# Optimization experiments

Measured on AMD Instinct MI355X. Metric: run time of the kernel, lower is better.

Reference implementation:

```python
import jax, jax.numpy as jnp
import numpy as np

N_NODES = 100000
N_EDGES = 1600000
F_IN = 64
F_OUT = 64


def setup_inputs() -> dict:
    key = jax.random.key(0)
    k1, k2, k3 = jax.random.split(key, 3)
    x = jax.random.normal(k1, (1, 1, N_NODES, F_IN), dtype=jnp.float32)
    edge_index = jax.random.randint(k2, (2, N_EDGES), 0, N_NODES, dtype=jnp.int32)
    # xavier-init linear weight [F_IN, F_OUT], zero bias (xavier_zero_bias)
    scale = jnp.sqrt(2.0 / (F_IN + F_OUT)).astype(jnp.float32)
    weight = jax.random.normal(k3, (F_IN, F_OUT), dtype=jnp.float32) * scale
    bias = jnp.zeros((F_OUT,), dtype=jnp.float32)
    return {"x": x, "edge_index": edge_index, "weight": weight, "bias": bias}


def reference(x, edge_index, weight, bias):
    # x: [B, T, N, F_in]
    B, T, N, _ = x.shape
    # linear transform
    h = jnp.einsum('btnf,fo->btno', x, weight) + bias  # [B,T,N,F_out]
    # add self loops
    loops = jnp.arange(N, dtype=edge_index.dtype)
    src = jnp.concatenate([edge_index[0], loops])  # [E+N]
    dst = jnp.concatenate([edge_index[1], loops])  # [E+N]
    w = jnp.ones(src.shape[0], dtype=h.dtype)
    # symmetric GCN normalization: D^{-1/2} A D^{-1/2} (degree over dst)
    deg = jnp.zeros((N,), dtype=h.dtype).at[dst].add(w)
    inv_sqrt = jnp.clip(deg, 1e-9) ** -0.5
    norm = inv_sqrt[dst] * w * inv_sqrt[src]  # [E+N]
    # gather src features, scale by norm, scatter-add to dst
    msg = h[:, :, src, :] * norm[None, None, :, None]  # [B,T,E+N,F_out]
    out = jnp.zeros_like(h).at[:, :, dst, :].add(msg)  # [B,T,N,F_out]
    # GraphConvBase post: activation (gelu), dropout=0, norm=identity
    return jax.nn.gelu(out)
```

## Files before the change

### kernel.cpp

```cpp
#include <hip/hip_runtime.h>
#include <hip/hip_fp16.h>
#include <math.h>

#define N_NODES 100000
#define N_EDGES 1600000
#define F_DIM 64
#define BSH 9
#define BNODES 512
#define NBUCK ((N_NODES + BNODES - 1) / BNODES)
#define CAP 12288
#define EPT 32
#define TILE (256 * EPT)
#define P1B ((N_EDGES + TILE - 1) / TILE)
#define LINB ((N_NODES + 255) / 256)

__global__ __launch_bounds__(256) void fused1_k(const int* __restrict__ src,
                                                const int* __restrict__ dst,
                                                int* __restrict__ bcur,
                                                unsigned int* __restrict__ tmp,
                                                const float* __restrict__ x,
                                                const float* __restrict__ W,
                                                const float* __restrict__ bias,
                                                __half* __restrict__ h) {
    if (blockIdx.x < P1B) {
        __shared__ int lcnt[NBUCK];
        __shared__ int lbase[NBUCK];
        for (int i = threadIdx.x; i < NBUCK; i += 256) lcnt[i] = 0;
        __syncthreads();

        int4 sreg[EPT / 4], dreg[EPT / 4];
        int base4 = blockIdx.x * (TILE / 4);
#pragma unroll
        for (int j = 0; j < EPT / 4; ++j) {
            int i4 = base4 + j * 256 + threadIdx.x;
            if (i4 < N_EDGES / 4) {
                sreg[j] = ((const int4*)src)[i4];
                dreg[j] = ((const int4*)dst)[i4];
                atomicAdd(&lcnt[dreg[j].x >> BSH], 1);
                atomicAdd(&lcnt[dreg[j].y >> BSH], 1);
                atomicAdd(&lcnt[dreg[j].z >> BSH], 1);
                atomicAdd(&lcnt[dreg[j].w >> BSH], 1);
            } else {
                dreg[j].x = -1;
            }
        }
        __syncthreads();
        for (int b = threadIdx.x; b < NBUCK; b += 256) {
            int c = lcnt[b];
            lbase[b] = c ? atomicAdd(&bcur[b], c) : 0;
            lcnt[b] = 0;
        }
        __syncthreads();
#pragma unroll
        for (int j = 0; j < EPT / 4; ++j) {
            if (dreg[j].x >= 0) {
                int d, s, b, r;
                d = dreg[j].x; s = sreg[j].x; b = d >> BSH;
                r = atomicAdd(&lcnt[b], 1);
                tmp[(size_t)b * CAP + lbase[b] + r] = (unsigned int)s | ((unsigned int)(d & (BNODES - 1)) << 17);
                d = dreg[j].y; s = sreg[j].y; b = d >> BSH;
                r = atomicAdd(&lcnt[b], 1);
                tmp[(size_t)b * CAP + lbase[b] + r] = (unsigned int)s | ((unsigned int)(d & (BNODES - 1)) << 17);
                d = dreg[j].z; s = sreg[j].z; b = d >> BSH;
                r = atomicAdd(&lcnt[b], 1);
                tmp[(size_t)b * CAP + lbase[b] + r] = (unsigned int)s | ((unsigned int)(d & (BNODES - 1)) << 17);
                d = dreg[j].w; s = sreg[j].w; b = d >> BSH;
                r = atomicAdd(&lcnt[b], 1);
                tmp[(size_t)b * CAP + lbase[b] + r] = (unsigned int)s | ((unsigned int)(d & (BNODES - 1)) << 17);
            }
        }
    } else {
        __shared__ float Ws[F_DIM][F_DIM];
        __shared__ float bs[F_DIM];
        for (int i = threadIdx.x; i < F_DIM * F_DIM; i += 256) Ws[i >> 6][i & 63] = W[i];
        if (threadIdx.x < F_DIM) bs[threadIdx.x] = bias[threadIdx.x];
        __syncthreads();

        int n = (blockIdx.x - P1B) * 256 + threadIdx.x;
        if (n >= N_NODES) return;

        float xr[F_DIM];
        const float4* xp = (const float4*)(x + (size_t)n * F_DIM);
#pragma unroll
        for (int k4 = 0; k4 < 16; ++k4) {
            float4 v = xp[k4];
            xr[k4 * 4 + 0] = v.x; xr[k4 * 4 + 1] = v.y;
            xr[k4 * 4 + 2] = v.z; xr[k4 * 4 + 3] = v.w;
        }
        __half* hp = h + (size_t)n * F_DIM;
#pragma unroll 1
        for (int f0 = 0; f0 < F_DIM; f0 += 4) {
            float a0 = bs[f0 + 0], a1 = bs[f0 + 1], a2 = bs[f0 + 2], a3 = bs[f0 + 3];
#pragma unroll
            for (int k = 0; k < F_DIM; ++k) {
                float xv = xr[k];
                a0 += xv * Ws[k][f0 + 0];
                a1 += xv * Ws[k][f0 + 1];
                a2 += xv * Ws[k][f0 + 2];
                a3 += xv * Ws[k][f0 + 3];
            }
            union { __half2 h2[2]; float2 f2; } u;
            u.h2[0] = __floats2half2_rn(a0, a1);
            u.h2[1] = __floats2half2_rn(a2, a3);
            *((float2*)(hp + f0)) = u.f2;
        }
    }
}

__global__ __launch_bounds__(1024) void passB_k(const unsigned int* __restrict__ tmp,
                                                const int* __restrict__ bcur,
                                                unsigned int* __restrict__ esrc,
                                                unsigned int* __restrict__ rowinfo,
                                                float* __restrict__ inv) {
    __shared__ int cnt[BNODES];
    __shared__ int cur[BNODES];
    __shared__ int ls[BNODES];
    int b = blockIdx.x;
    int tid = threadIdx.x;
    int beg0 = b * CAP;
    int cntb = bcur[b];

    if (tid < BNODES) cnt[tid] = 0;
    __syncthreads();
    for (int i = tid; i < cntb; i += 1024)
        atomicAdd(&cnt[tmp[beg0 + i] >> 17], 1);
    __syncthreads();

    int a = 0;
    if (tid < BNODES) { a = cnt[tid]; ls[tid] = a; }
    __syncthreads();
    for (int off = 1; off < BNODES; off <<= 1) {
        int p = 0;
        if (tid < BNODES && tid >= off) p = ls[tid - off];
        __syncthreads();
        if (tid < BNODES) ls[tid] += p;
        __syncthreads();
    }
    if (tid < BNODES) {
        int p0 = beg0 + ls[tid] - a;
        cur[tid] = p0;
        int n = (b << BSH) + tid;
        if (n < N_NODES) {
            rowinfo[n] = (unsigned int)p0 | ((unsigned int)a << 22);
            inv[n] = rsqrtf((float)(a + 1));
        }
    }
    __syncthreads();

    for (int i = tid; i < cntb; i += 1024) {
        unsigned int v = tmp[beg0 + i];
        int pos = atomicAdd(&cur[v >> 17], 1);
        esrc[pos] = v & 0x1FFFFu;
    }
}

__device__ __forceinline__ float gelu1(float x) {
    float x3 = x * x * x;
    float t = tanhf(0.7978845608028654f * (x + 0.044715f * x3));
    return 0.5f * x * (1.0f + t);
}

__global__ __launch_bounds__(256) void gather_k(const __half* __restrict__ h,
                                                const float* __restrict__ inv,
                                                const unsigned int* __restrict__ rowinfo,
                                                const unsigned int* __restrict__ esrc,
                                                float* __restrict__ out, int N) {
    int n = blockIdx.x * 4 + (threadIdx.x >> 6);
    if (n >= N) return;
    int lane = threadIdx.x & 63;
    int eslot = lane >> 4;
    int fq = lane & 15;

    unsigned int ri = rowinfo[n];
    int beg = (int)(ri & 0x3FFFFFu);
    int deg = (int)(ri >> 22);

    float ax = 0.f, ay = 0.f, az = 0.f, aw = 0.f;
    int k = eslot;
    for (; k + 12 < deg; k += 16) {
        int s0 = (int)esrc[beg + k];
        int s1 = (int)esrc[beg + k + 4];
        int s2 = (int)esrc[beg + k + 8];
        int s3 = (int)esrc[beg + k + 12];
        float w0 = inv[s0], w1 = inv[s1], w2 = inv[s2], w3 = inv[s3];
        union { float2 f; __half2 h2[2]; } u0, u1, u2, u3;
        u0.f = *((const float2*)(h + (size_t)s0 * F_DIM) + fq);
        u1.f = *((const float2*)(h + (size_t)s1 * F_DIM) + fq);
        u2.f = *((const float2*)(h + (size_t)s2 * F_DIM) + fq);
        u3.f = *((const float2*)(h + (size_t)s3 * F_DIM) + fq);
        float2 a, b;
        a = __half22float2(u0.h2[0]); b = __half22float2(u0.h2[1]);
        ax = fmaf(a.x, w0, ax); ay = fmaf(a.y, w0, ay); az = fmaf(b.x, w0, az); aw = fmaf(b.y, w0, aw);
        a = __half22float2(u1.h2[0]); b = __half22float2(u1.h2[1]);
        ax = fmaf(a.x, w1, ax); ay = fmaf(a.y, w1, ay); az = fmaf(b.x, w1, az); aw = fmaf(b.y, w1, aw);
        a = __half22float2(u2.h2[0]); b = __half22float2(u2.h2[1]);
        ax = fmaf(a.x, w2, ax); ay = fmaf(a.y, w2, ay); az = fmaf(b.x, w2, az); aw = fmaf(b.y, w2, aw);
        a = __half22float2(u3.h2[0]); b = __half22float2(u3.h2[1]);
        ax = fmaf(a.x, w3, ax); ay = fmaf(a.y, w3, ay); az = fmaf(b.x, w3, az); aw = fmaf(b.y, w3, aw);
    }
    for (; k < deg; k += 4) {
        int s0 = (int)esrc[beg + k];
        float w0 = inv[s0];
        union { float2 f; __half2 h2[2]; } u0;
        u0.f = *((const float2*)(h + (size_t)s0 * F_DIM) + fq);
        float2 a = __half22float2(u0.h2[0]);
        float2 b = __half22float2(u0.h2[1]);
        ax = fmaf(a.x, w0, ax); ay = fmaf(a.y, w0, ay); az = fmaf(b.x, w0, az); aw = fmaf(b.y, w0, aw);
    }
    ax += __shfl_xor(ax, 16); ay += __shfl_xor(ay, 16);
    az += __shfl_xor(az, 16); aw += __shfl_xor(aw, 16);
    ax += __shfl_xor(ax, 32); ay += __shfl_xor(ay, 32);
    az += __shfl_xor(az, 32); aw += __shfl_xor(aw, 32);

    if (eslot == 0) {
        float invn = inv[n];
        union { float2 f; __half2 h2[2]; } us;
        us.f = *((const float2*)(h + (size_t)n * F_DIM) + fq);
        float2 s0 = __half22float2(us.h2[0]);
        float2 s1 = __half22float2(us.h2[1]);
        float4 o;
        o.x = gelu1((ax + s0.x * invn) * invn);
        o.y = gelu1((ay + s0.y * invn) * invn);
        o.z = gelu1((az + s1.x * invn) * invn);
        o.w = gelu1((aw + s1.y * invn) * invn);
        ((float4*)(out + (size_t)n * F_DIM))[fq] = o;
    }
}

extern "C" void kernel_launch(void* const* d_in, const int* in_sizes, int n_in,
                              void* d_out, int out_size, void* d_ws, size_t ws_size,
                              hipStream_t stream) {
    const float* x    = (const float*)d_in[0];
    const int*   ei   = (const int*)d_in[1];
    const float* W    = (const float*)d_in[2];
    const float* bias = (const float*)d_in[3];
    float* out = (float*)d_out;

    const int* src = ei;
    const int* dst = ei + N_EDGES;

    unsigned int* tmp     = (unsigned int*)d_ws;
    unsigned int* esrc    = tmp + (size_t)NBUCK * CAP;
    unsigned int* rowinfo = esrc + (size_t)NBUCK * CAP;
    float*        inv     = (float*)(rowinfo + N_NODES);
    int*          bcur    = (int*)(inv + N_NODES);
    size_t off = (size_t)(bcur + NBUCK) - (size_t)d_ws;
    off = (off + 31) & ~(size_t)31;
    __half* h = (__half*)((char*)d_ws + off);

    hipMemsetAsync(bcur, 0, NBUCK * sizeof(int), stream);

    fused1_k<<<P1B + LINB, 256, 0, stream>>>(src, dst, bcur, tmp, x, W, bias, h);
    passB_k<<<NBUCK, 1024, 0, stream>>>(tmp, bcur, esrc, rowinfo, inv);
    gather_k<<<(N_NODES + 3) / 4, 256, 0, stream>>>(h, inv, rowinfo, esrc, out, N_NODES);
}
```

Baseline: 113.8 us.

## Merge bucket-sort second pass into first kernel via grid-wide atomic barrier

```diff
diff --git a/kernel.cpp b/kernel.cpp
--- a/kernel.cpp
+++ b/kernel.cpp
@@ -13,26 +13,42 @@
 #define TILE (256 * EPT)
 #define P1B ((N_EDGES + TILE - 1) / TILE)
 #define LINB ((N_NODES + 255) / 256)
-
-__global__ __launch_bounds__(256) void fused1_k(const int* __restrict__ src,
-                                                const int* __restrict__ dst,
-                                                int* __restrict__ bcur,
-                                                unsigned int* __restrict__ tmp,
-                                                const float* __restrict__ x,
-                                                const float* __restrict__ W,
-                                                const float* __restrict__ bias,
-                                                __half* __restrict__ h) {
-    if (blockIdx.x < P1B) {
-        __shared__ int lcnt[NBUCK];
-        __shared__ int lbase[NBUCK];
-        for (int i = threadIdx.x; i < NBUCK; i += 256) lcnt[i] = 0;
+#define GRID (P1B + LINB)
+
+typedef float __attribute__((ext_vector_type(4))) f32x4;
+
+__global__ __launch_bounds__(256, 4) void fusedall_k(const int* __restrict__ src,
+                                                     const int* __restrict__ dst,
+                                                     int* __restrict__ bcur,
+                                                     unsigned int* __restrict__ tmp,
+                                                     const float* __restrict__ x,
+                                                     const float* __restrict__ W,
+                                                     const float* __restrict__ bias,
+                                                     __half* __restrict__ h,
+                                                     unsigned int* __restrict__ esrc,
+                                                     unsigned int* __restrict__ rowinfo,
+                                                     float* __restrict__ inv) {
+    __shared__ int lcnt[NBUCK];
+    __shared__ int lbase[NBUCK];
+    __shared__ float Ws[F_DIM][F_DIM];
+    __shared__ float bs[F_DIM];
+    __shared__ int cnt[BNODES];
+    __shared__ int cur[BNODES];
+    __shared__ int ls[256];
+
+    const int bid = blockIdx.x;
+    const int tid = threadIdx.x;
+    int* done = bcur + NBUCK;
+
+    if (bid < P1B) {
+        for (int i = tid; i < NBUCK; i += 256) lcnt[i] = 0;
         __syncthreads();
 
         int4 sreg[EPT / 4], dreg[EPT / 4];
-        int base4 = blockIdx.x * (TILE / 4);
+        int base4 = bid * (TILE / 4);
 #pragma unroll
         for (int j = 0; j < EPT / 4; ++j) {
-            int i4 = base4 + j * 256 + threadIdx.x;
+            int i4 = base4 + j * 256 + tid;
             if (i4 < N_EDGES / 4) {
                 sreg[j] = ((const int4*)src)[i4];
                 dreg[j] = ((const int4*)dst)[i4];
@@ -45,7 +61,7 @@
             }
         }
         __syncthreads();
-        for (int b = threadIdx.x; b < NBUCK; b += 256) {
+        for (int b = tid; b < NBUCK; b += 256) {
             int c = lcnt[b];
             lbase[b] = c ? atomicAdd(&bcur[b], c) : 0;
             lcnt[b] = 0;
@@ -70,87 +86,98 @@
             }
         }
     } else {
-        __shared__ float Ws[F_DIM][F_DIM];
-        __shared__ float bs[F_DIM];
-        for (int i = threadIdx.x; i < F_DIM * F_DIM; i += 256) Ws[i >> 6][i & 63] = W[i];
-        if (threadIdx.x < F_DIM) bs[threadIdx.x] = bias[threadIdx.x];
-        __syncthreads();
-
-        int n = (blockIdx.x - P1B) * 256 + threadIdx.x;
-        if (n >= N_NODES) return;
-
-        float xr[F_DIM];
-        const float4* xp = (const float4*)(x + (size_t)n * F_DIM);
-#pragma unroll
-        for (int k4 = 0; k4 < 16; ++k4) {
-            float4 v = xp[k4];
-            xr[k4 * 4 + 0] = v.x; xr[k4 * 4 + 1] = v.y;
-            xr[k4 * 4 + 2] = v.z; xr[k4 * 4 + 3] = v.w;
-        }
-        __half* hp = h + (size_t)n * F_DIM;
+        for (int i = tid; i < F_DIM * F_DIM; i += 256) Ws[i >> 6][i & 63] = W[i];
+        if (tid < F_DIM) bs[tid] = bias[tid];
+        __syncthreads();
+
+        int n = (bid - P1B) * 256 + tid;
+        if (n < N_NODES) {
+            float xr[F_DIM];
+            const float4* xp = (const float4*)(x + (size_t)n * F_DIM);
+#pragma unroll
+            for (int k4 = 0; k4 < 16; ++k4) {
+                float4 v = xp[k4];
+                xr[k4 * 4 + 0] = v.x; xr[k4 * 4 + 1] = v.y;
+                xr[k4 * 4 + 2] = v.z; xr[k4 * 4 + 3] = v.w;
+            }
+            __half* hp = h + (size_t)n * F_DIM;
 #pragma unroll 1
-        for (int f0 = 0; f0 < F_DIM; f0 += 4) {
-            float a0 = bs[f0 + 0], a1 = bs[f0 + 1], a2 = bs[f0 + 2], a3 = bs[f0 + 3];
-#pragma unroll
-            for (int k = 0; k < F_DIM; ++k) {
-                float xv = xr[k];
-                a0 += xv * Ws[k][f0 + 0];
-                a1 += xv * Ws[k][f0 + 1];
-                a2 += xv * Ws[k][f0 + 2];
-                a3 += xv * Ws[k][f0 + 3];
-            }
-            union { __half2 h2[2]; float2 f2; } u;
-            u.h2[0] = __floats2half2_rn(a0, a1);
-            u.h2[1] = __floats2half2_rn(a2, a3);
-            *((float2*)(hp + f0)) = u.f2;
-        }
-    }
-}
-
-__global__ __launch_bounds__(1024) void passB_k(const unsigned int* __restrict__ tmp,
-                                                const int* __restrict__ bcur,
-                                                unsigned int* __restrict__ esrc,
-                                                unsigned int* __restrict__ rowinfo,
-                                                float* __restrict__ inv) {
-    __shared__ int cnt[BNODES];
-    __shared__ int cur[BNODES];
-    __shared__ int ls[BNODES];
-    int b = blockIdx.x;
-    int tid = threadIdx.x;
-    int beg0 = b * CAP;
-    int cntb = bcur[b];
-
-    if (tid < BNODES) cnt[tid] = 0;
+            for (int f0 = 0; f0 < F_DIM; f0 += 4) {
+                float a0 = bs[f0 + 0], a1 = bs[f0 + 1], a2 = bs[f0 + 2], a3 = bs[f0 + 3];
+#pragma unroll
+                for (int k = 0; k < F_DIM; ++k) {
+                    float xv = xr[k];
+                    a0 += xv * Ws[k][f0 + 0];
+                    a1 += xv * Ws[k][f0 + 1];
+                    a2 += xv * Ws[k][f0 + 2];
+                    a3 += xv * Ws[k][f0 + 3];
+                }
+                union { __half2 h2[2]; float2 f2; } u;
+                u.h2[0] = __floats2half2_rn(a0, a1);
+                u.h2[1] = __floats2half2_rn(a2, a3);
+                *((float2*)(hp + f0)) = u.f2;
+            }
+        }
+    }
+
+    __threadfence();
     __syncthreads();
-    for (int i = tid; i < cntb; i += 1024)
-        atomicAdd(&cnt[tmp[beg0 + i] >> 17], 1);
+    if (tid == 0)
+        __hip_atomic_fetch_add(done, 1, __ATOMIC_RELEASE, __HIP_MEMORY_SCOPE_AGENT);
+
+    if (bid >= NBUCK) return;
+
+    if (tid == 0) {
+        while (__hip_atomic_load(done, __ATOMIC_ACQUIRE, __HIP_MEMORY_SCOPE_AGENT) < GRID)
+            __builtin_amdgcn_s_sleep(2);
+    }
     __syncthreads();
-
-    int a = 0;
-    if (tid < BNODES) { a = cnt[tid]; ls[tid] = a; }
-    __syncthreads();
-    for (int off = 1; off < BNODES; off <<= 1) {
-        int p = 0;
-        if (tid < BNODES && tid >= off) p = ls[tid - off];
-        __syncthreads();
-        if (tid < BNODES) ls[tid] += p;
-        __syncthreads();
-    }
-    if (tid < BNODES) {
-        int p0 = beg0 + ls[tid] - a;
-        cur[tid] = p0;
-        int n = (b << BSH) + tid;
-        if (n < N_NODES) {
-            rowinfo[n] = (unsigned int)p0 | ((unsigned int)a << 22);
-            inv[n] = rsqrtf((float)(a + 1));
-        }
-    }
-    __syncthreads();
-
-    for (int i = tid; i < cntb; i += 1024) {
-        unsigned int v = tmp[beg0 + i];
-        int pos = atomicAdd(&cur[v >> 17], 1);
-        esrc[pos] = v & 0x1FFFFu;
+    __threadfence();
+
+    {
+        int b = bid;
+        int beg0 = b * CAP;
+        int cntb = bcur[b];
+
+        cnt[tid] = 0;
+        cnt[tid + 256] = 0;
+        __syncthreads();
+        for (int i = tid; i < cntb; i += 256)
+            atomicAdd(&cnt[tmp[beg0 + i] >> 17], 1);
+        __syncthreads();
+
+        int a0 = cnt[2 * tid];
+        int a1 = cnt[2 * tid + 1];
+        int tsum = a0 + a1;
+        ls[tid] = tsum;
+        __syncthreads();
+        for (int off = 1; off < 256; off <<= 1) {
+            int p = (tid >= off) ? ls[tid - off] : 0;
+            __syncthreads();
+            ls[tid] += p;
+            __syncthreads();
+        }
+        int excl = ls[tid] - tsum;
+        int p0 = beg0 + excl;
+        int p1 = p0 + a0;
+        cur[2 * tid] = p0;
+        cur[2 * tid + 1] = p1;
+        int n0 = (b << BSH) + 2 * tid;
+        if (n0 < N_NODES) {
+            rowinfo[n0] = (unsigned int)p0 | ((unsigned int)a0 << 22);
+            inv[n0] = rsqrtf((float)(a0 + 1));
+        }
+        if (n0 + 1 < N_NODES) {
+            rowinfo[n0 + 1] = (unsigned int)p1 | ((unsigned int)a1 << 22);
+            inv[n0 + 1] = rsqrtf((float)(a1 + 1));
+        }
+        __syncthreads();
+
+        for (int i = tid; i < cntb; i += 256) {
+            unsigned int v = tmp[beg0 + i];
+            int pos = atomicAdd(&cur[v >> 17], 1);
+            esrc[pos] = v & 0x1FFFFu;
+        }
     }
 }
 
@@ -244,13 +271,12 @@
     unsigned int* rowinfo = esrc + (size_t)NBUCK * CAP;
     float*        inv     = (float*)(rowinfo + N_NODES);
     int*          bcur    = (int*)(inv + N_NODES);
-    size_t off = (size_t)(bcur + NBUCK) - (size_t)d_ws;
+    size_t off = (size_t)(bcur + NBUCK + 1) - (size_t)d_ws;
     off = (off + 31) & ~(size_t)31;
     __half* h = (__half*)((char*)d_ws + off);
 
-    hipMemsetAsync(bcur, 0, NBUCK * sizeof(int), stream);
-
-    fused1_k<<<P1B + LINB, 256, 0, stream>>>(src, dst, bcur, tmp, x, W, bias, h);
-    passB_k<<<NBUCK, 1024, 0, stream>>>(tmp, bcur, esrc, rowinfo, inv);
+    hipMemsetAsync(bcur, 0, (NBUCK + 1) * sizeof(int), stream);
+
+    fusedall_k<<<GRID, 256, 0, stream>>>(src, dst, bcur, tmp, x, W, bias, h, esrc, rowinfo, inv);
     gather_k<<<(N_NODES + 3) / 4, 256, 0, stream>>>(h, inv, rowinfo, esrc, out, N_NODES);
 }
```

Measured after the change: 436.1 us. +283.2%, slower.
